# Kernel tuning notes

Hardware: AMD Instinct MI355X
Metric: run time of the kernel (lower is better)

The kernel has to match this reference:

```python
import jax, jax.numpy as jnp
import numpy as np

B, N, T, FD = 128, 64, 20, 2
E, H, A = 16, 32, 32
DB, DH = 30.0, 30.0
NB, NHD = 12, 12  # 360/30 bearing and heading bins
DOMAIN_INIT = 5.0
EPS = 1e-12


def setup_inputs() -> dict:
    key = jax.random.key(0)
    ks = jax.random.split(key, 20)
    rn = lambda k, s, sc=0.1: (jax.random.normal(k, s) * sc).astype(jnp.float32)
    return {
        'x': jax.random.normal(ks[0], (B, N, T, FD), jnp.float32),
        'dmat': jax.random.uniform(ks[1], (B, N, T, N), jnp.float32) * 10.0,
        'bmat': jax.random.uniform(ks[2], (B, N, T, N), jnp.float32) * 360.0,
        'hmat': jax.random.uniform(ks[3], (B, N, T, N), jnp.float32) * 360.0,
        'mask': jnp.ones((B, N, T), jnp.float32),
        'emb_W': rn(ks[4], (E, FD)), 'emb_b': rn(ks[5], (E,)),
        'W_ih': rn(ks[6], (4 * H, E)), 'W_hh': rn(ks[7], (4 * H, H)),
        'b_ih': rn(ks[8], (4 * H,)), 'b_hh': rn(ks[9], (4 * H,)),
        'domain': jnp.full((NB, NHD), DOMAIN_INIT, jnp.float32),
        'enc2att_W': rn(ks[10], (A, H)), 'enc2att_b': rn(ks[11], (A,)),
        'spa_W': rn(ks[12], (A, 2 * A)), 'spa_b': rn(ks[13], (A,)),
        'att2enc_W': rn(ks[14], (H, A)), 'att2enc_b': rn(ks[15], (H,)),
        'cls_W': rn(ks[16], (1, H)), 'cls_b': rn(ks[17], (1,)),
        'h0': jax.random.normal(ks[18], (B * N, H), jnp.float32),
        'c0': jax.random.normal(ks[19], (B * N, H), jnp.float32),
    }


def _forward(x, dmat, bmat, hmat, mask, emb_W, emb_b, W_ih, W_hh, b_ih, b_hh,
             domain, enc2att_W, enc2att_b, spa_W, spa_b, att2enc_W, att2enc_b,
             cls_W, cls_b, h0, c0):
    # input embedding: [B,N,T,F] -> [T, B*N, E] (time-major for scan)
    xe = jnp.einsum('bntf,ef->bnte', x, emb_W) + emb_b
    xe = jnp.moveaxis(xe.reshape(B * N, T, E), 1, 0)
    dm_t = jnp.moveaxis(dmat, 2, 0)   # [T,B,N,N]
    bm_t = jnp.moveaxis(bmat, 2, 0)
    hm_t = jnp.moveaxis(hmat, 2, 0)
    mk_t = jnp.moveaxis(mask, 2, 0)   # [T,B,N]
    eye = jnp.eye(N, dtype=x.dtype)

    def step(carry, inputs):
        h, c = carry                     # [B*N, H]
        xt, dm, bm, hm, mk = inputs
        # single-step LSTM cell (torch gate order i,f,g,o)
        g = xt @ W_ih.T + b_ih + h @ W_hh.T + b_hh
        i, f, gg, o = jnp.split(g, 4, axis=-1)
        c = jax.nn.sigmoid(f) * c + jax.nn.sigmoid(i) * jnp.tanh(gg)
        h = jax.nn.sigmoid(o) * jnp.tanh(c)
        # project encoder state to attention space: [B,N,A]
        a = h.reshape(B, N, H) @ enc2att_W.T + enc2att_b
        # spatial attention weights from distance/bearing/heading edge feats
        ib = jnp.clip(jnp.floor(bm / DB), 0, NB - 1).astype(jnp.int32)
        ih = jnp.clip(jnp.floor(hm / DH), 0, NHD - 1).astype(jnp.int32)
        w = jax.nn.relu(domain[ib, ih] - dm)               # [B,N,N]
        w = w * mk[:, :, None] * mk[:, None, :] * (1.0 - eye)
        w = w / (jnp.sum(w, axis=-1, keepdims=True) + EPS)
        att = jnp.einsum('bij,bjd->bid', w, a)
        z = jnp.tanh(jnp.concatenate([a, att], axis=-1) @ spa_W.T + spa_b)
        h = (z @ att2enc_W.T + att2enc_b).reshape(B * N, H)
        return (h, c), None

    (h, c), _ = jax.lax.scan(step, (h0, c0), (xe, dm_t, bm_t, hm_t, mk_t))
    scores = jnp.tanh(h.reshape(B, N, H) @ cls_W.T + cls_b)
    return jax.nn.sigmoid(scores)  # [B, N, 1]


def reference(x, dmat, bmat, hmat, mask, emb_W, emb_b, W_ih, W_hh, b_ih, b_hh,
              domain, enc2att_W, enc2att_b, spa_W, spa_b, att2enc_W, att2enc_b,
              cls_W, cls_b, h0, c0):
    return _forward(x, dmat, bmat, hmat, mask, emb_W, emb_b, W_ih, W_hh, b_ih,
                    b_hh, domain, enc2att_W, enc2att_b, spa_W, spa_b,
                    att2enc_W, att2enc_b, cls_W, cls_b, h0, c0)
```

## Files before the change

### kernel.cpp

```cpp
#include <hip/hip_runtime.h>
#include <math.h>

#define T_STEPS 20

typedef _Float16 half8 __attribute__((ext_vector_type(8)));
typedef _Float16 half4v __attribute__((ext_vector_type(4)));
typedef float f32x4 __attribute__((ext_vector_type(4)));

__device__ __forceinline__ float sigm(float v) {
  return __builtin_amdgcn_rcpf(1.0f + __expf(-v));
}
__device__ __forceinline__ float tanh_f(float v) {
  return 1.0f - 2.0f * __builtin_amdgcn_rcpf(1.0f + __expf(2.0f * v));
}

__global__ __launch_bounds__(1024)
void traj_disc(const float* __restrict__ x, const float* __restrict__ dmat,
               const float* __restrict__ bmat, const float* __restrict__ hmat,
               const float* __restrict__ maskp,
               const float* __restrict__ embW, const float* __restrict__ embb,
               const float* __restrict__ Wih, const float* __restrict__ Whh,
               const float* __restrict__ bih, const float* __restrict__ bhh,
               const float* __restrict__ dom,
               const float* __restrict__ e2aW, const float* __restrict__ e2ab,
               const float* __restrict__ spaW, const float* __restrict__ spab,
               const float* __restrict__ a2eW, const float* __restrict__ a2eb,
               const float* __restrict__ clsW, const float* __restrict__ clsb,
               const float* __restrict__ h0p, const float* __restrict__ c0p,
               float* __restrict__ out)
{
  __shared__ __align__(16) _Float16 sgw[128*40];
  __shared__ __align__(16) float4   sgmb[128];
  __shared__ __align__(16) _Float16 sESaT[32*40];
  __shared__ __align__(16) _Float16 sEStT[32*40];
  __shared__ __align__(16) _Float16 sa2e[32*40];
  __shared__ float bz[32];
  __shared__ float sa2eb[32];
  __shared__ float sdom[144];
  __shared__ float sm[1280];
  __shared__ float sclsW[32];
  __shared__ float sclsb;
  __shared__ __align__(16) _Float16 sH[64*40];
  __shared__ __align__(16) _Float16 sw[64*72];
  __shared__ __align__(16) _Float16 sz_[64*40];
  __shared__ __align__(16) _Float16 sQT[32*72];
  __shared__ __align__(16) float sgates[128*68];

  const int tid = threadIdx.x;
  const int b = blockIdx.x;
  const int i = tid >> 4;
  const int s = tid & 15;
  const int w = tid >> 6;
  const int l = tid & 63;
  const int quad = l >> 4;
  const int n16 = l & 15;

  for (int idx = tid; idx < 4096; idx += 1024) sgw[(idx >> 5)*40 + (idx & 31)] = (_Float16)Whh[idx];
  if (tid < 128) {
    float m0 = 0.f, m1 = 0.f, bb = bih[tid] + bhh[tid];
    #pragma unroll
    for (int e = 0; e < 16; ++e) {
      float wv_ = Wih[tid*16 + e];
      m0 = fmaf(wv_, embW[2*e],   m0);
      m1 = fmaf(wv_, embW[2*e+1], m1);
      bb = fmaf(wv_, embb[e],     bb);
    }
    sgmb[tid] = make_float4(m0, m1, bb, 0.f);
  }
  {
    const int zk = tid >> 5, hc = tid & 31;
    float sa_ = 0.f, st_ = 0.f;
    #pragma unroll
    for (int a = 0; a < 32; ++a) {
      const float ev = e2aW[a*32 + hc];
      sa_ = fmaf(spaW[zk*64 + a],      ev, sa_);
      st_ = fmaf(spaW[zk*64 + 32 + a], ev, st_);
    }
    sESaT[zk*40 + hc] = (_Float16)sa_;
    sEStT[zk*40 + hc] = (_Float16)st_;
  }
  for (int idx = tid; idx < 1024; idx += 1024) sa2e[(idx >> 5)*40 + (idx & 31)] = (_Float16)a2eW[idx];
  if (tid < 32) {
    float acc = spab[tid];
    #pragma unroll
    for (int a = 0; a < 32; ++a)
      acc = fmaf(e2ab[a], spaW[tid*64 + a] + spaW[tid*64 + 32 + a], acc);
    bz[tid] = acc;
    sa2eb[tid] = a2eb[tid];
    sclsW[tid] = clsW[tid];
  }
  if (tid < 144) sdom[tid] = dom[tid];
  if (tid == 0) sclsb = clsb[0];
  for (int idx = tid; idx < 1280; idx += 1024) sm[idx] = maskp[(size_t)b*1280 + idx];
  for (int idx = tid; idx < 2048; idx += 1024) sH[(idx >> 5)*40 + (idx & 31)] = (_Float16)h0p[(size_t)b*2048 + idx];
  float c0r = c0p[(size_t)b*2048 + i*32 + s];
  float c1r = c0p[(size_t)b*2048 + i*32 + s + 16];
  __syncthreads();

  const size_t nb = (size_t)b*64 + i;

  #pragma unroll 1
  for (int t = 0; t < T_STEPS; ++t) {
    const size_t ebase = (nb*20 + t)*64;
#define EDGELD(jj) const float dm##jj = dmat[ebase + s + 16*(jj)]; \
                   const float bm##jj = bmat[ebase + s + 16*(jj)]; \
                   const float hm##jj = hmat[ebase + s + 16*(jj)];
    EDGELD(0) EDGELD(1) EDGELD(2) EDGELD(3)
#undef EDGELD

    {
      const int r1 = w >> 2, cp = (w & 3) << 1;
      const half8 Af = *(const half8*)(sH + (16*r1 + n16)*40 + quad*8);
      const float* xb = x + (((size_t)b*64 + 16*r1 + 4*quad)*20 + t)*2;
      const float2 xA = *(const float2*)(xb +   0);
      const float2 xB = *(const float2*)(xb +  40);
      const float2 xC = *(const float2*)(xb +  80);
      const float2 xD = *(const float2*)(xb + 120);
#define OP1C(c) { \
      const half8 Bf = *(const half8*)(sgw + (16*(c) + n16)*40 + quad*8); \
      const float4 mb = sgmb[16*(c) + n16]; \
      f32x4 Cv; \
      Cv[0] = fmaf(xA.x, mb.x, fmaf(xA.y, mb.y, mb.z)); \
      Cv[1] = fmaf(xB.x, mb.x, fmaf(xB.y, mb.y, mb.z)); \
      Cv[2] = fmaf(xC.x, mb.x, fmaf(xC.y, mb.y, mb.z)); \
      Cv[3] = fmaf(xD.x, mb.x, fmaf(xD.y, mb.y, mb.z)); \
      Cv = __builtin_amdgcn_mfma_f32_16x16x32_f16(Af, Bf, Cv, 0, 0, 0); \
      *(f32x4*)(sgates + (16*(c) + n16)*68 + 16*r1 + 4*quad) = Cv; }
      OP1C(cp) OP1C(cp + 1)
#undef OP1C
    }
    __syncthreads();

    {
#define GR(q, u) sgates[((q)*32 + s + 16*(u))*68 + i]
      const float ai0 = GR(0,0), af0 = GR(1,0), ag0 = GR(2,0), ao0 = GR(3,0);
      const float ai1 = GR(0,1), af1 = GR(1,1), ag1 = GR(2,1), ao1 = GR(3,1);
#undef GR
      c0r = fmaf(sigm(af0), c0r, sigm(ai0)*tanh_f(ag0));
      sH[i*40 + s]      = (_Float16)(sigm(ao0)*tanh_f(c0r));
      c1r = fmaf(sigm(af1), c1r, sigm(ai1)*tanh_f(ag1));
      sH[i*40 + s + 16] = (_Float16)(sigm(ao1)*tanh_f(c1r));
    }
    {
      const float mi_ = sm[i*20 + t];
      float rs = 0.0f;
#define WCOMP(jj) float wn##jj; { \
      int ib_ = (int)floorf(bm##jj * (1.0f/30.0f)); ib_ = ib_ < 0 ? 0 : (ib_ > 11 ? 11 : ib_); \
      int ih_ = (int)floorf(hm##jj * (1.0f/30.0f)); ih_ = ih_ < 0 ? 0 : (ih_ > 11 ? 11 : ih_); \
      float w_ = fmaxf(sdom[ib_*12 + ih_] - dm##jj, 0.0f) * (mi_ * sm[(s + 16*(jj))*20 + t]); \
      wn##jj = (s + 16*(jj) == i) ? 0.0f : w_; rs += wn##jj; }
      WCOMP(0) WCOMP(1) WCOMP(2) WCOMP(3)
#undef WCOMP
      rs += __shfl_xor(rs, 1); rs += __shfl_xor(rs, 2);
      rs += __shfl_xor(rs, 4); rs += __shfl_xor(rs, 8);
      const float inv_ = __builtin_amdgcn_rcpf(rs + 1e-12f);
      sw[i*72 + s +  0] = (_Float16)(wn0 * inv_);
      sw[i*72 + s + 16] = (_Float16)(wn1 * inv_);
      sw[i*72 + s + 32] = (_Float16)(wn2 * inv_);
      sw[i*72 + s + 48] = (_Float16)(wn3 * inv_);
    }
    __syncthreads();

    if (w < 8) {
      const int r = w >> 1, c = w & 1;
      const half8 Af = *(const half8*)(sH    + (16*r + n16)*40 + quad*8);
      const half8 Bf = *(const half8*)(sESaT + (16*c + n16)*40 + quad*8);
      f32x4 Cv = {0.f, 0.f, 0.f, 0.f};
      Cv = __builtin_amdgcn_mfma_f32_16x16x32_f16(Af, Bf, Cv, 0, 0, 0);
      *(f32x4*)(sgates + (16*c + n16)*68 + 16*r + 4*quad) = Cv;
    } else {
      const int w8 = w - 8, r = w8 >> 1, c = w8 & 1;
      const half8 Af = *(const half8*)(sH    + (16*r + n16)*40 + quad*8);
      const half8 Bf = *(const half8*)(sEStT + (16*c + n16)*40 + quad*8);
      f32x4 Cv = {0.f, 0.f, 0.f, 0.f};
      Cv = __builtin_amdgcn_mfma_f32_16x16x32_f16(Af, Bf, Cv, 0, 0, 0);
      half4v hq;
      hq[0] = (_Float16)Cv[0]; hq[1] = (_Float16)Cv[1];
      hq[2] = (_Float16)Cv[2]; hq[3] = (_Float16)Cv[3];
      *(half4v*)(sQT + (16*c + n16)*72 + 16*r + 4*quad) = hq;
    }
    __syncthreads();

    if (w >= 8) {
      const int w8 = w - 8, r = w8 >> 1, c = w8 & 1;
      const half8 A0 = *(const half8*)(sw  + (16*r + n16)*72 + quad*8);
      const half8 A1 = *(const half8*)(sw  + (16*r + n16)*72 + 32 + quad*8);
      const half8 B0 = *(const half8*)(sQT + (16*c + n16)*72 + quad*8);
      const half8 B1 = *(const half8*)(sQT + (16*c + n16)*72 + 32 + quad*8);
      const f32x4 Pv = *(const f32x4*)(sgates + (16*c + n16)*68 + 16*r + 4*quad);
      const float bzv = bz[16*c + n16];
      f32x4 Cv;
      Cv[0] = Pv[0] + bzv; Cv[1] = Pv[1] + bzv;
      Cv[2] = Pv[2] + bzv; Cv[3] = Pv[3] + bzv;
      Cv = __builtin_amdgcn_mfma_f32_16x16x32_f16(A0, B0, Cv, 0, 0, 0);
      Cv = __builtin_amdgcn_mfma_f32_16x16x32_f16(A1, B1, Cv, 0, 0, 0);
      const int nd = 16*r + 4*quad;
      sz_[(nd+0)*40 + 16*c + n16] = (_Float16)tanh_f(Cv[0]);
      sz_[(nd+1)*40 + 16*c + n16] = (_Float16)tanh_f(Cv[1]);
      sz_[(nd+2)*40 + 16*c + n16] = (_Float16)tanh_f(Cv[2]);
      sz_[(nd+3)*40 + 16*c + n16] = (_Float16)tanh_f(Cv[3]);
    }
    __syncthreads();

    if (w < 8) {
      const int r = w >> 1, c = w & 1;
      const half8 Af = *(const half8*)(sz_  + (16*r + n16)*40 + quad*8);
      const half8 Bf = *(const half8*)(sa2e + (16*c + n16)*40 + quad*8);
      const float bv = sa2eb[16*c + n16];
      f32x4 Cv = {bv, bv, bv, bv};
      Cv = __builtin_amdgcn_mfma_f32_16x16x32_f16(Af, Bf, Cv, 0, 0, 0);
      const int nd = 16*r + 4*quad;
      sH[(nd+0)*40 + 16*c + n16] = (_Float16)Cv[0];
      sH[(nd+1)*40 + 16*c + n16] = (_Float16)Cv[1];
      sH[(nd+2)*40 + 16*c + n16] = (_Float16)Cv[2];
      sH[(nd+3)*40 + 16*c + n16] = (_Float16)Cv[3];
    }
    __syncthreads();
  }

  if (tid < 64) {
    float acc = sclsb;
    #pragma unroll
    for (int hh = 0; hh < 32; ++hh) acc = fmaf((float)sH[tid*40 + hh], sclsW[hh], acc);
    out[(size_t)b*64 + tid] = sigm(tanh_f(acc));
  }
}

extern "C" void kernel_launch(void* const* d_in, const int* in_sizes, int n_in,
                              void* d_out, int out_size, void* d_ws, size_t ws_size,
                              hipStream_t stream) {
  (void)in_sizes; (void)n_in; (void)d_ws; (void)ws_size; (void)out_size;
  const float* x    = (const float*)d_in[0];
  const float* dmat = (const float*)d_in[1];
  const float* bmat = (const float*)d_in[2];
  const float* hmat = (const float*)d_in[3];
  const float* mask = (const float*)d_in[4];
  const float* embW = (const float*)d_in[5];
  const float* embb = (const float*)d_in[6];
  const float* Wih  = (const float*)d_in[7];
  const float* Whh  = (const float*)d_in[8];
  const float* bih  = (const float*)d_in[9];
  const float* bhh  = (const float*)d_in[10];
  const float* dom  = (const float*)d_in[11];
  const float* e2aW = (const float*)d_in[12];
  const float* e2ab = (const float*)d_in[13];
  const float* spaW = (const float*)d_in[14];
  const float* spab = (const float*)d_in[15];
  const float* a2eW = (const float*)d_in[16];
  const float* a2eb = (const float*)d_in[17];
  const float* clsW = (const float*)d_in[18];
  const float* clsb = (const float*)d_in[19];
  const float* h0   = (const float*)d_in[20];
  const float* c0   = (const float*)d_in[21];
  float* out = (float*)d_out;

  traj_disc<<<dim3(128), dim3(1024), 0, stream>>>(
      x, dmat, bmat, hmat, mask, embW, embb, Wih, Whh, bih, bhh, dom,
      e2aW, e2ab, spaW, spab, a2eW, a2eb, clsW, clsb, h0, c0, out);
}
```

Baseline: 238.4 us.

## Fold att2enc projection into recurrent and classifier weights, prefetch edge inputs

Precomputes Whh·a2eW and the matching bias so each step feeds z straight into the next LSTM gate matmul, and folds a2eW into the classifier weights. This removes one MFMA stage and one barrier per time step. The first step still uses h0 with the original Whh. It also keeps Pv in registers instead of a shared-memory round trip, reassigns the spatial matmul to the same warps, and prefetches next-step edge and x data before the barrier. Folding the weights in fp16 changes rounding slightly.

```diff
diff --git a/kernel.cpp b/kernel.cpp
--- a/kernel.cpp
+++ b/kernel.cpp
@@ -30,16 +30,15 @@
                float* __restrict__ out)
 {
   __shared__ __align__(16) _Float16 sgw[128*40];
+  __shared__ __align__(16) _Float16 sgwc[128*40];
   __shared__ __align__(16) float4   sgmb[128];
   __shared__ __align__(16) _Float16 sESaT[32*40];
   __shared__ __align__(16) _Float16 sEStT[32*40];
-  __shared__ __align__(16) _Float16 sa2e[32*40];
   __shared__ float bz[32];
-  __shared__ float sa2eb[32];
   __shared__ float sdom[144];
   __shared__ float sm[1280];
-  __shared__ float sclsW[32];
-  __shared__ float sclsb;
+  __shared__ float sclsc[32];
+  __shared__ float sclsb2[1];
   __shared__ __align__(16) _Float16 sH[64*40];
   __shared__ __align__(16) _Float16 sw[64*72];
   __shared__ __align__(16) _Float16 sz_[64*40];
@@ -56,16 +55,33 @@
   const int n16 = l & 15;
 
   for (int idx = tid; idx < 4096; idx += 1024) sgw[(idx >> 5)*40 + (idx & 31)] = (_Float16)Whh[idx];
+  {
+    const int g = tid >> 3, kb = (tid & 7) << 2;
+    float a0 = 0.f, a1 = 0.f, a2 = 0.f, a3 = 0.f;
+    #pragma unroll
+    for (int h = 0; h < 32; ++h) {
+      const float wv = Whh[g*32 + h];
+      a0 = fmaf(wv, a2eW[h*32 + kb + 0], a0);
+      a1 = fmaf(wv, a2eW[h*32 + kb + 1], a1);
+      a2 = fmaf(wv, a2eW[h*32 + kb + 2], a2);
+      a3 = fmaf(wv, a2eW[h*32 + kb + 3], a3);
+    }
+    sgwc[g*40 + kb + 0] = (_Float16)a0; sgwc[g*40 + kb + 1] = (_Float16)a1;
+    sgwc[g*40 + kb + 2] = (_Float16)a2; sgwc[g*40 + kb + 3] = (_Float16)a3;
+  }
   if (tid < 128) {
-    float m0 = 0.f, m1 = 0.f, bb = bih[tid] + bhh[tid];
+    float m0 = 0.f, m1 = 0.f, b0 = bih[tid] + bhh[tid];
     #pragma unroll
     for (int e = 0; e < 16; ++e) {
       float wv_ = Wih[tid*16 + e];
       m0 = fmaf(wv_, embW[2*e],   m0);
       m1 = fmaf(wv_, embW[2*e+1], m1);
-      bb = fmaf(wv_, embb[e],     bb);
-    }
-    sgmb[tid] = make_float4(m0, m1, bb, 0.f);
+      b0 = fmaf(wv_, embb[e],     b0);
+    }
+    float bn = b0;
+    #pragma unroll
+    for (int h = 0; h < 32; ++h) bn = fmaf(Whh[tid*32 + h], a2eb[h], bn);
+    sgmb[tid] = make_float4(m0, m1, b0, bn);
   }
   {
     const int zk = tid >> 5, hc = tid & 31;
@@ -79,18 +95,24 @@
     sESaT[zk*40 + hc] = (_Float16)sa_;
     sEStT[zk*40 + hc] = (_Float16)st_;
   }
-  for (int idx = tid; idx < 1024; idx += 1024) sa2e[(idx >> 5)*40 + (idx & 31)] = (_Float16)a2eW[idx];
   if (tid < 32) {
     float acc = spab[tid];
     #pragma unroll
     for (int a = 0; a < 32; ++a)
       acc = fmaf(e2ab[a], spaW[tid*64 + a] + spaW[tid*64 + 32 + a], acc);
     bz[tid] = acc;
-    sa2eb[tid] = a2eb[tid];
-    sclsW[tid] = clsW[tid];
+    float cc = 0.f;
+    #pragma unroll
+    for (int h = 0; h < 32; ++h) cc = fmaf(clsW[h], a2eW[h*32 + tid], cc);
+    sclsc[tid] = cc;
+  }
+  if (tid == 0) {
+    float cb = clsb[0];
+    #pragma unroll
+    for (int h = 0; h < 32; ++h) cb = fmaf(clsW[h], a2eb[h], cb);
+    sclsb2[0] = cb;
   }
   if (tid < 144) sdom[tid] = dom[tid];
-  if (tid == 0) sclsb = clsb[0];
   for (int idx = tid; idx < 1280; idx += 1024) sm[idx] = maskp[(size_t)b*1280 + idx];
   for (int idx = tid; idx < 2048; idx += 1024) sH[(idx >> 5)*40 + (idx & 31)] = (_Float16)h0p[(size_t)b*2048 + idx];
   float c0r = c0p[(size_t)b*2048 + i*32 + s];
@@ -99,31 +121,33 @@
 
   const size_t nb = (size_t)b*64 + i;
 
+  const float* xpre = x + (size_t)(b*64 + ((w >> 2) << 4) + (quad << 2)) * 40;
+  float2 xA = *(const float2*)(xpre +   0);
+  float2 xB = *(const float2*)(xpre +  40);
+  float2 xC = *(const float2*)(xpre +  80);
+  float2 xD = *(const float2*)(xpre + 120);
+  size_t eb_ = nb*1280;
+  float dm0 = dmat[eb_ + s],      bm0 = bmat[eb_ + s],      hm0 = hmat[eb_ + s];
+  float dm1 = dmat[eb_ + s + 16], bm1 = bmat[eb_ + s + 16], hm1 = hmat[eb_ + s + 16];
+  float dm2 = dmat[eb_ + s + 32], bm2 = bmat[eb_ + s + 32], hm2 = hmat[eb_ + s + 32];
+  float dm3 = dmat[eb_ + s + 48], bm3 = bmat[eb_ + s + 48], hm3 = hmat[eb_ + s + 48];
+
   #pragma unroll 1
   for (int t = 0; t < T_STEPS; ++t) {
-    const size_t ebase = (nb*20 + t)*64;
-#define EDGELD(jj) const float dm##jj = dmat[ebase + s + 16*(jj)]; \
-                   const float bm##jj = bmat[ebase + s + 16*(jj)]; \
-                   const float hm##jj = hmat[ebase + s + 16*(jj)];
-    EDGELD(0) EDGELD(1) EDGELD(2) EDGELD(3)
-#undef EDGELD
-
     {
       const int r1 = w >> 2, cp = (w & 3) << 1;
-      const half8 Af = *(const half8*)(sH + (16*r1 + n16)*40 + quad*8);
-      const float* xb = x + (((size_t)b*64 + 16*r1 + 4*quad)*20 + t)*2;
-      const float2 xA = *(const float2*)(xb +   0);
-      const float2 xB = *(const float2*)(xb +  40);
-      const float2 xC = *(const float2*)(xb +  80);
-      const float2 xD = *(const float2*)(xb + 120);
+      const _Float16* Abase = (t == 0) ? sH : sz_;
+      const _Float16* Bbase = (t == 0) ? sgw : sgwc;
+      const half8 Af = *(const half8*)(Abase + (16*r1 + n16)*40 + quad*8);
 #define OP1C(c) { \
-      const half8 Bf = *(const half8*)(sgw + (16*(c) + n16)*40 + quad*8); \
+      const half8 Bf = *(const half8*)(Bbase + (16*(c) + n16)*40 + quad*8); \
       const float4 mb = sgmb[16*(c) + n16]; \
+      const float bb = (t == 0) ? mb.z : mb.w; \
       f32x4 Cv; \
-      Cv[0] = fmaf(xA.x, mb.x, fmaf(xA.y, mb.y, mb.z)); \
-      Cv[1] = fmaf(xB.x, mb.x, fmaf(xB.y, mb.y, mb.z)); \
-      Cv[2] = fmaf(xC.x, mb.x, fmaf(xC.y, mb.y, mb.z)); \
-      Cv[3] = fmaf(xD.x, mb.x, fmaf(xD.y, mb.y, mb.z)); \
+      Cv[0] = fmaf(xA.x, mb.x, fmaf(xA.y, mb.y, bb)); \
+      Cv[1] = fmaf(xB.x, mb.x, fmaf(xB.y, mb.y, bb)); \
+      Cv[2] = fmaf(xC.x, mb.x, fmaf(xC.y, mb.y, bb)); \
+      Cv[3] = fmaf(xD.x, mb.x, fmaf(xD.y, mb.y, bb)); \
       Cv = __builtin_amdgcn_mfma_f32_16x16x32_f16(Af, Bf, Cv, 0, 0, 0); \
       *(f32x4*)(sgates + (16*(c) + n16)*68 + 16*r1 + 4*quad) = Cv; }
       OP1C(cp) OP1C(cp + 1)
@@ -159,15 +183,29 @@
       sw[i*72 + s + 32] = (_Float16)(wn2 * inv_);
       sw[i*72 + s + 48] = (_Float16)(wn3 * inv_);
     }
-    __syncthreads();
-
+    {
+      const int tn = (t < T_STEPS - 1) ? t + 1 : t;
+      const size_t ebn = (nb*20 + tn)*64;
+      dm0 = dmat[ebn + s];      bm0 = bmat[ebn + s];      hm0 = hmat[ebn + s];
+      dm1 = dmat[ebn + s + 16]; bm1 = bmat[ebn + s + 16]; hm1 = hmat[ebn + s + 16];
+      dm2 = dmat[ebn + s + 32]; bm2 = bmat[ebn + s + 32]; hm2 = hmat[ebn + s + 32];
+      dm3 = dmat[ebn + s + 48]; bm3 = bmat[ebn + s + 48]; hm3 = hmat[ebn + s + 48];
+      const int tn2 = tn << 1;
+      xA = *(const float2*)(xpre + tn2);
+      xB = *(const float2*)(xpre + tn2 +  40);
+      xC = *(const float2*)(xpre + tn2 +  80);
+      xD = *(const float2*)(xpre + tn2 + 120);
+    }
+    __syncthreads();
+
+    f32x4 Pv = {0.f, 0.f, 0.f, 0.f};
     if (w < 8) {
       const int r = w >> 1, c = w & 1;
       const half8 Af = *(const half8*)(sH    + (16*r + n16)*40 + quad*8);
       const half8 Bf = *(const half8*)(sESaT + (16*c + n16)*40 + quad*8);
-      f32x4 Cv = {0.f, 0.f, 0.f, 0.f};
-      Cv = __builtin_amdgcn_mfma_f32_16x16x32_f16(Af, Bf, Cv, 0, 0, 0);
-      *(f32x4*)(sgates + (16*c + n16)*68 + 16*r + 4*quad) = Cv;
+      const float bzv = bz[16*c + n16];
+      Pv[0] = bzv; Pv[1] = bzv; Pv[2] = bzv; Pv[3] = bzv;
+      Pv = __builtin_amdgcn_mfma_f32_16x16x32_f16(Af, Bf, Pv, 0, 0, 0);
     } else {
       const int w8 = w - 8, r = w8 >> 1, c = w8 & 1;
       const half8 Af = *(const half8*)(sH    + (16*r + n16)*40 + quad*8);
@@ -181,47 +219,27 @@
     }
     __syncthreads();
 
-    if (w >= 8) {
-      const int w8 = w - 8, r = w8 >> 1, c = w8 & 1;
+    if (w < 8) {
+      const int r = w >> 1, c = w & 1;
       const half8 A0 = *(const half8*)(sw  + (16*r + n16)*72 + quad*8);
       const half8 A1 = *(const half8*)(sw  + (16*r + n16)*72 + 32 + quad*8);
       const half8 B0 = *(const half8*)(sQT + (16*c + n16)*72 + quad*8);
       const half8 B1 = *(const half8*)(sQT + (16*c + n16)*72 + 32 + quad*8);
-      const f32x4 Pv = *(const f32x4*)(sgates + (16*c + n16)*68 + 16*r + 4*quad);
-      const float bzv = bz[16*c + n16];
-      f32x4 Cv;
-      Cv[0] = Pv[0] + bzv; Cv[1] = Pv[1] + bzv;
-      Cv[2] = Pv[2] + bzv; Cv[3] = Pv[3] + bzv;
-      Cv = __builtin_amdgcn_mfma_f32_16x16x32_f16(A0, B0, Cv, 0, 0, 0);
-      Cv = __builtin_amdgcn_mfma_f32_16x16x32_f16(A1, B1, Cv, 0, 0, 0);
+      Pv = __builtin_amdgcn_mfma_f32_16x16x32_f16(A0, B0, Pv, 0, 0, 0);
+      Pv = __builtin_amdgcn_mfma_f32_16x16x32_f16(A1, B1, Pv, 0, 0, 0);
       const int nd = 16*r + 4*quad;
-      sz_[(nd+0)*40 + 16*c + n16] = (_Float16)tanh_f(Cv[0]);
-      sz_[(nd+1)*40 + 16*c + n16] = (_Float16)tanh_f(Cv[1]);
-      sz_[(nd+2)*40 + 16*c + n16] = (_Float16)tanh_f(Cv[2]);
-      sz_[(nd+3)*40 + 16*c + n16] = (_Float16)tanh_f(Cv[3]);
-    }
-    __syncthreads();
-
-    if (w < 8) {
-      const int r = w >> 1, c = w & 1;
-      const half8 Af = *(const half8*)(sz_  + (16*r + n16)*40 + quad*8);
-      const half8 Bf = *(const half8*)(sa2e + (16*c + n16)*40 + quad*8);
-      const float bv = sa2eb[16*c + n16];
-      f32x4 Cv = {bv, bv, bv, bv};
-      Cv = __builtin_amdgcn_mfma_f32_16x16x32_f16(Af, Bf, Cv, 0, 0, 0);
-      const int nd = 16*r + 4*quad;
-      sH[(nd+0)*40 + 16*c + n16] = (_Float16)Cv[0];
-      sH[(nd+1)*40 + 16*c + n16] = (_Float16)Cv[1];
-      sH[(nd+2)*40 + 16*c + n16] = (_Float16)Cv[2];
-      sH[(nd+3)*40 + 16*c + n16] = (_Float16)Cv[3];
+      sz_[(nd+0)*40 + 16*c + n16] = (_Float16)tanh_f(Pv[0]);
+      sz_[(nd+1)*40 + 16*c + n16] = (_Float16)tanh_f(Pv[1]);
+      sz_[(nd+2)*40 + 16*c + n16] = (_Float16)tanh_f(Pv[2]);
+      sz_[(nd+3)*40 + 16*c + n16] = (_Float16)tanh_f(Pv[3]);
     }
     __syncthreads();
   }
 
   if (tid < 64) {
-    float acc = sclsb;
-    #pragma unroll
-    for (int hh = 0; hh < 32; ++hh) acc = fmaf((float)sH[tid*40 + hh], sclsW[hh], acc);
+    float acc = sclsb2[0];
+    #pragma unroll
+    for (int k = 0; k < 32; ++k) acc = fmaf((float)sz_[tid*40 + k], sclsc[k], acc);
     out[(size_t)b*64 + tid] = sigm(tanh_f(acc));
   }
 }
```

After: 225.0 us. -5.6%, faster.
